# Performance work log

Measured on AMD Instinct MI355X. Metric: run time of the kernel, lower is better.

Reference implementation:

```python
import jax, jax.numpy as jnp
import numpy as np

H, NOPE, ROPE, VDIM, LORA = 16, 128, 64, 128, 512
DM, T, S, K = 2048, 256, 32768, 2048
SCALE = 1.0 / np.sqrt(NOPE + ROPE)
ROPE_BASE = 10000.0


def _rope(x, pos):
    # x: [..., D] with rotary dim D; pos broadcastable to x[..., :1] leading dims
    d = x.shape[-1]
    half = d // 2
    inv = 1.0 / (ROPE_BASE ** (jnp.arange(half, dtype=jnp.float32) / half))
    f = pos[..., None].astype(jnp.float32) * inv  # [..., half]
    cos, sin = jnp.cos(f), jnp.sin(f)
    x1, x2 = x[..., :half], x[..., half:]
    return jnp.concatenate([x1 * cos - x2 * sin, x2 * cos + x1 * sin], axis=-1)


def setup_inputs() -> dict:
    key = jax.random.key(0)
    ks = jax.random.split(key, 9)
    return {
        "x": jax.random.normal(ks[0], (T, DM), jnp.float32) * 0.02,
        "Wq": jax.random.normal(ks[1], (DM, H * (NOPE + ROPE)), jnp.float32) * 0.02,
        "W_UK": jax.random.normal(ks[2], (H, NOPE, LORA), jnp.float32) * 0.02,
        "W_UV": jax.random.normal(ks[3], (H, VDIM, LORA), jnp.float32) * 0.02,
        "Wo": jax.random.normal(ks[4], (H * VDIM, DM), jnp.float32) * 0.02,
        "kv_c": jax.random.normal(ks[5], (S, LORA), jnp.float32),
        "k_pe": jax.random.normal(ks[6], (S, ROPE), jnp.float32),
        "topk_indices": jnp.sort(jax.random.randint(ks[7], (T, K), 0, S, jnp.int32), axis=-1),
        "pos_q": jax.random.randint(ks[8], (T,), 0, S, jnp.int32),
    }


def reference(x, Wq, W_UK, W_UV, Wo, kv_c, k_pe, topk_indices, pos_q):
    n_tok = x.shape[0]
    # q projection -> [T, H, nope+rope], split (MLAAttention._q_proj_and_k_up_proj)
    q = (x @ Wq).reshape(n_tok, H, NOPE + ROPE)
    q_nope, q_pe = q[..., :NOPE], q[..., NOPE:]
    # absorbed k up-projection: q_nope @ W_UK -> latent space [T, H, LORA]
    ql_nope = jnp.einsum("thn,hnl->thl", q_nope, W_UK)
    # rotary on rope parts
    q_pe = _rope(q_pe, pos_q[:, None])            # [T, H, ROPE]
    k_pe_r = _rope(k_pe, jnp.arange(k_pe.shape[0]))  # [S, ROPE]
    # top-k sparse KV gather (DSA indexer / triton index conversion)
    kv_sel = kv_c[topk_indices]                    # [T, K, LORA]
    kpe_sel = k_pe_r[topk_indices]                 # [T, K, ROPE]
    # attention scores in latent space over selected tokens
    scores = (jnp.einsum("thl,tkl->thk", ql_nope, kv_sel)
              + jnp.einsum("thr,tkr->thk", q_pe, kpe_sel)) * SCALE
    attn = jax.nn.softmax(scores, axis=-1)         # [T, H, K]
    o_lat = jnp.einsum("thk,tkl->thl", attn, kv_sel)  # [T, H, LORA]
    # v up-projection (_v_up_proj_and_o_proj) then output proj
    ov = jnp.einsum("thl,hvl->thv", o_lat, W_UV).reshape(n_tok, H * VDIM)
    return ov @ Wo
```

## Files before the change

kernel.cpp:

```cpp
#include <hip/hip_runtime.h>
#include <hip/hip_bf16.h>

#define H_    16
#define NOPE_ 128
#define ROPE_ 64
#define VDIM_ 128
#define LORA_ 512
#define DM_   2048
#define T_    256
#define S_    32768
#define K_    2048

static constexpr float SCALE_ = 0.072168783648703220563643597562744f;
static constexpr float LOG2E_ = 1.4426950408889634f;

typedef __attribute__((ext_vector_type(8))) short short8;
typedef __attribute__((ext_vector_type(4))) short short4v;
typedef __attribute__((ext_vector_type(4))) float f32x4;

__device__ __forceinline__ ushort f2bf(float f) {
    unsigned u = __float_as_uint(f);
    unsigned r = (u + 0x7FFFu + ((u >> 16) & 1u)) >> 16;
    return (ushort)r;
}
__device__ __forceinline__ float bf2f(ushort u) {
    return __uint_as_float((unsigned)u << 16);
}

template<bool A_BF16, bool B_NT, bool C_BF16, bool SMALL_M>
__global__ __launch_bounds__(256) void gemm_mfma(
    const void* __restrict__ Av, const float* __restrict__ B, void* __restrict__ Cv,
    int M, int N, int Kd, int lda, int ldb, int ldc,
    long batchA, long batchB, long batchC)
{
    constexpr int BM = SMALL_M ? 32 : 64;
    constexpr int MT = SMALL_M ? 1 : 2;
    __shared__ ushort As[64 * 72];
    __shared__ ushort Bs[64 * 72];

    const int tid = threadIdx.x;
    const int w  = tid >> 6;
    const int l  = tid & 63;
    const int lm = l & 15;
    const int kq = l >> 4;
    const int bm = blockIdx.y * BM;
    const int bn = blockIdx.x * 64;
    const int m0 = SMALL_M ? (w >> 1) * 16 : (w >> 1) * 32;
    const int n0 = (w & 1) * 32;

    const float*  Af = A_BF16 ? nullptr : ((const float*)Av)  + (long)blockIdx.z * batchA;
    const ushort* Ah = A_BF16 ? ((const ushort*)Av) + (long)blockIdx.z * batchA : nullptr;
    B += (long)blockIdx.z * batchB;

    f32x4 acc[MT][2];
    #pragma unroll
    for (int i = 0; i < MT; ++i)
        #pragma unroll
        for (int j = 0; j < 2; ++j) acc[i][j] = (f32x4){0.f, 0.f, 0.f, 0.f};

    const int am  = SMALL_M ? (tid >> 3) : (tid >> 2);
    const int ako = SMALL_M ? (tid & 7) * 8 : (tid & 3) * 16;
    const int amr = SMALL_M ? (tid >> 3) : (tid >> 4);
    const int akk = SMALL_M ? (tid & 7) * 8 : (tid & 15) * 4;
    const int bnr = tid >> 4, bkk = (tid & 15) * 4;
    const int bk  = tid >> 2, bnq = (tid & 3) * 16;

    uint4  gA[2];
    float4 gAf[4];
    float4 gB[4];

    auto loadA = [&](int k0) {
        if constexpr (A_BF16) {
            const ushort* src = Ah + (long)(bm + am) * lda + k0 + ako;
            gA[0] = *(const uint4*)(src);
            if constexpr (!SMALL_M) gA[1] = *(const uint4*)(src + 8);
        } else {
            if constexpr (SMALL_M) {
                const float* s = Af + (long)(bm + amr) * lda + k0 + akk;
                gAf[0] = *(const float4*)s;
                gAf[1] = *(const float4*)(s + 4);
            } else {
                #pragma unroll
                for (int p = 0; p < 4; ++p)
                    gAf[p] = *(const float4*)(Af + (long)(bm + amr + p * 16) * lda + k0 + akk);
            }
        }
    };
    auto loadB = [&](int k0) {
        if constexpr (B_NT) {
            #pragma unroll
            for (int p = 0; p < 4; ++p)
                gB[p] = *(const float4*)(B + (long)(bn + bnr + p * 16) * ldb + k0 + bkk);
        } else {
            #pragma unroll
            for (int p = 0; p < 4; ++p)
                gB[p] = *(const float4*)(B + (long)(k0 + bk) * ldb + bn + bnq + p * 4);
        }
    };

    loadA(0); loadB(0);

    for (int k0 = 0; k0 < Kd; k0 += 64) {
        __syncthreads();
        if constexpr (A_BF16) {
            *(uint4*)(As + am * 72 + ako) = gA[0];
            if constexpr (!SMALL_M)
                *(uint4*)(As + am * 72 + ako + 8) = gA[1];
        } else {
            if constexpr (SMALL_M) {
                ushort4 u0, u1;
                u0.x = f2bf(gAf[0].x); u0.y = f2bf(gAf[0].y);
                u0.z = f2bf(gAf[0].z); u0.w = f2bf(gAf[0].w);
                u1.x = f2bf(gAf[1].x); u1.y = f2bf(gAf[1].y);
                u1.z = f2bf(gAf[1].z); u1.w = f2bf(gAf[1].w);
                *(ushort4*)(As + amr * 72 + akk)     = u0;
                *(ushort4*)(As + amr * 72 + akk + 4) = u1;
            } else {
                #pragma unroll
                for (int p = 0; p < 4; ++p) {
                    ushort4 u;
                    u.x = f2bf(gAf[p].x); u.y = f2bf(gAf[p].y);
                    u.z = f2bf(gAf[p].z); u.w = f2bf(gAf[p].w);
                    *(ushort4*)(As + (amr + p * 16) * 72 + akk) = u;
                }
            }
        }
        if constexpr (B_NT) {
            #pragma unroll
            for (int p = 0; p < 4; ++p) {
                ushort4 u;
                u.x = f2bf(gB[p].x); u.y = f2bf(gB[p].y);
                u.z = f2bf(gB[p].z); u.w = f2bf(gB[p].w);
                *(ushort4*)(Bs + (bnr + p * 16) * 72 + bkk) = u;
            }
        } else {
            #pragma unroll
            for (int p = 0; p < 4; ++p) {
                ushort4 u;
                u.x = f2bf(gB[p].x); u.y = f2bf(gB[p].y);
                u.z = f2bf(gB[p].z); u.w = f2bf(gB[p].w);
                *(ushort4*)(Bs + bk * 68 + bnq + p * 4) = u;
            }
        }
        if (k0 + 64 < Kd) { loadA(k0 + 64); loadB(k0 + 64); }
        __syncthreads();
        #pragma unroll
        for (int ks = 0; ks < 2; ++ks) {
            short8 a[MT], b[2];
            #pragma unroll
            for (int mt = 0; mt < MT; ++mt)
                a[mt] = *(const short8*)(As + (m0 + mt * 16 + lm) * 72 + ks * 32 + kq * 8);
            if constexpr (B_NT) {
                #pragma unroll
                for (int nt = 0; nt < 2; ++nt)
                    b[nt] = *(const short8*)(Bs + (n0 + nt * 16 + lm) * 72 + ks * 32 + kq * 8);
            } else {
                #pragma unroll
                for (int nt = 0; nt < 2; ++nt)
                    #pragma unroll
                    for (int j = 0; j < 8; ++j)
                        b[nt][j] = (short)Bs[(ks * 32 + kq * 8 + j) * 68 + n0 + nt * 16 + lm];
            }
            #pragma unroll
            for (int mt = 0; mt < MT; ++mt)
                #pragma unroll
                for (int nt = 0; nt < 2; ++nt)
                    acc[mt][nt] = __builtin_amdgcn_mfma_f32_16x16x32_bf16(
                        a[mt], b[nt], acc[mt][nt], 0, 0, 0);
        }
    }
    #pragma unroll
    for (int mt = 0; mt < MT; ++mt)
        #pragma unroll
        for (int nt = 0; nt < 2; ++nt)
            #pragma unroll
            for (int r = 0; r < 4; ++r) {
                long row = bm + m0 + mt * 16 + kq * 4 + r;
                long col = bn + n0 + nt * 16 + lm;
                if constexpr (C_BF16)
                    ((ushort*)Cv)[(long)blockIdx.z * batchC + row * ldc + col] =
                        f2bf(acc[mt][nt][r]);
                else
                    ((float*)Cv)[(long)blockIdx.z * batchC + row * ldc + col] =
                        acc[mt][nt][r];
            }
}

__global__ __launch_bounds__(256) void pack_qrope(
    const float* __restrict__ qfull, const int* __restrict__ pos_q,
    ushort* __restrict__ qb)
{
    int id = blockIdx.x * 256 + threadIdx.x;
    int i = id & 31;
    int h = (id >> 5) & 15;
    int t = id >> 9;
    double inv = exp2(-(double)i * 0.41524101186092026);
    double f = (double)pos_q[t] * inv;
    double fr = f - floor(f * 0.15915494309189535) * 6.283185307179586;
    float sf, cf;
    sincosf((float)fr, &sf, &cf);
    float x1 = qfull[t * 3072 + h * 192 + 128 + i];
    float x2 = qfull[t * 3072 + h * 192 + 160 + i];
    ushort* q = qb + (long)(t * 16 + h) * 576;
    q[512 + i] = f2bf(x1 * cf - x2 * sf);
    q[544 + i] = f2bf(x2 * cf + x1 * sf);
}

__global__ __launch_bounds__(256) void prep_kvb(
    const float* __restrict__ kvc, const float* __restrict__ kpe,
    ushort* __restrict__ kvb)
{
    int id = blockIdx.x * 256 + threadIdx.x;
    int s = id / 96;
    int c = id - s * 96;
    if (c < 64) {
        const float* src = kvc + (long)s * 512 + c * 8;
        float4 v0 = *(const float4*)src;
        float4 v1 = *(const float4*)(src + 4);
        ushort4 a, b;
        a.x = f2bf(v0.x); a.y = f2bf(v0.y); a.z = f2bf(v0.z); a.w = f2bf(v0.w);
        b.x = f2bf(v1.x); b.y = f2bf(v1.y); b.z = f2bf(v1.z); b.w = f2bf(v1.w);
        ushort* dst = kvb + (long)s * 576 + c * 8;
        *(ushort4*)dst = a;
        *(ushort4*)(dst + 4) = b;
    } else {
        int i = c - 64;
        double inv = exp2(-(double)i * 0.41524101186092026);
        double f = (double)s * inv;
        double fr = f - floor(f * 0.15915494309189535) * 6.283185307179586;
        float sf, cf;
        sincosf((float)fr, &sf, &cf);
        const float* kp = kpe + (long)s * 64;
        float x1 = kp[i], x2 = kp[32 + i];
        ushort* dst = kvb + (long)s * 576 + 512;
        dst[i]      = f2bf(x1 * cf - x2 * sf);
        dst[32 + i] = f2bf(x2 * cf + x1 * sf);
    }
}

#define KBD 2048
#define KBSZ 73728

__global__ __launch_bounds__(256, 4) void mla_fused_split(
    const ushort* __restrict__ qb, const ushort* __restrict__ kvb,
    const int* __restrict__ topk,
    ushort* __restrict__ Opart, float* __restrict__ ml)
{
    __shared__ __align__(16) char kb[KBSZ];
    __shared__ __align__(16) ushort P2[1024];
    __shared__ float wred[2][4][16];

    const int t = blockIdx.x;
    const int sp = blockIdx.y;
    const int tid = threadIdx.x;
    const int w = tid >> 6;
    const int l = tid & 63;
    const int lm = l & 15;
    const int kq = l >> 4;

    short8 qa[18];
    {
        const ushort* qrow = qb + (long)(t * 16 + lm) * 576 + kq * 8;
        #pragma unroll
        for (int ks = 0; ks < 18; ++ks)
            qa[ks] = *(const short8*)(qrow + ks * 32);
    }

    const int* tkp = topk + (long)t * 2048 + sp * 1024;

    const int kh   = w & 1;
    const int db0  = w >> 1;
    const int skey = 32 * kh + (l >> 1);
    const int gcol = db0 * 16 + (l & 1) * 8;
    const unsigned stRel = (unsigned)(db0 * 2048 + kh * 1024);

    __attribute__((address_space(3))) char* kb3 =
        (__attribute__((address_space(3))) char*)&kb[0];
    const char* kbg = (const char*)&kb[0];
    const unsigned kbBase = (unsigned)(unsigned long long)(const void*)&kb[0];

    const unsigned krowRel = (unsigned)((kq >> 1) * KBD + w * 512 + (lm >> 2) * 128
                     + (lm & 3) * 32 + (kq & 1) * 16);
    const unsigned trb = kbBase + (unsigned)(w * 8 * KBD + kq * 256 + lm * 8);
    const unsigned ptrb = (unsigned)(unsigned long long)(const void*)P2
                        + (unsigned)(kq * 256 + lm * 8);

    f32x4 O[8];
    #pragma unroll
    for (int vt = 0; vt < 8; ++vt) O[vt] = (f32x4){0.f, 0.f, 0.f, 0.f};
    float m_r[4] = {-1e30f, -1e30f, -1e30f, -1e30f};
    float l_r[4] = {0.f, 0.f, 0.f, 0.f};

#define GSTAGE(IDX)                                                           \
    {                                                                         \
        const ushort* gs = kvb + (long)(IDX) * 576 + gcol;                    \
        _Pragma("unroll")                                                     \
        for (int i = 0; i < 18; ++i)                                          \
            __builtin_amdgcn_global_load_lds(                                 \
                (const __attribute__((address_space(1))) void*)(const void*)(gs + i * 32), \
                (__attribute__((address_space(3))) void*)(kb3 + stRel + i * 4096), \
                16, 0, 0);                                                    \
    }

    for (int tt = 0; tt < 16; ++tt) {
        int idx = tkp[tt * 64 + skey];
        __syncthreads();
        GSTAGE(idx)

        const char* krow = kbg + krowRel;
        f32x4 S0 = (f32x4){0.f, 0.f, 0.f, 0.f};
        f32x4 S1 = (f32x4){0.f, 0.f, 0.f, 0.f};

        asm volatile("s_waitcnt vmcnt(12)" ::: "memory");
        __builtin_amdgcn_s_barrier();
        asm volatile("" ::: "memory");
        #pragma unroll
        for (int ks = 0; ks < 6; ks += 2) {
            short8 b0 = *(const short8*)(krow + ks * (2 * KBD));
            S0 = __builtin_amdgcn_mfma_f32_16x16x32_bf16(qa[ks], b0, S0, 0, 0, 0);
            short8 b1 = *(const short8*)(krow + (ks + 1) * (2 * KBD));
            S1 = __builtin_amdgcn_mfma_f32_16x16x32_bf16(qa[ks + 1], b1, S1, 0, 0, 0);
        }
        asm volatile("s_waitcnt vmcnt(6)" ::: "memory");
        __builtin_amdgcn_s_barrier();
        asm volatile("" ::: "memory");
        #pragma unroll
        for (int ks = 6; ks < 12; ks += 2) {
            short8 b0 = *(const short8*)(krow + ks * (2 * KBD));
            S0 = __builtin_amdgcn_mfma_f32_16x16x32_bf16(qa[ks], b0, S0, 0, 0, 0);
            short8 b1 = *(const short8*)(krow + (ks + 1) * (2 * KBD));
            S1 = __builtin_amdgcn_mfma_f32_16x16x32_bf16(qa[ks + 1], b1, S1, 0, 0, 0);
        }
        asm volatile("s_waitcnt vmcnt(0)" ::: "memory");
        __builtin_amdgcn_s_barrier();
        asm volatile("" ::: "memory");
        #pragma unroll
        for (int ks = 12; ks < 18; ks += 2) {
            short8 b0 = *(const short8*)(krow + ks * (2 * KBD));
            S0 = __builtin_amdgcn_mfma_f32_16x16x32_bf16(qa[ks], b0, S0, 0, 0, 0);
            short8 b1 = *(const short8*)(krow + (ks + 1) * (2 * KBD));
            S1 = __builtin_amdgcn_mfma_f32_16x16x32_bf16(qa[ks + 1], b1, S1, 0, 0, 0);
        }

        float s4[4], mx[4], p[4];
        #pragma unroll
        for (int r = 0; r < 4; ++r) { s4[r] = (S0[r] + S1[r]) * SCALE_; mx[r] = s4[r]; }
        #pragma unroll
        for (int off = 1; off < 16; off <<= 1)
            #pragma unroll
            for (int r = 0; r < 4; ++r)
                mx[r] = fmaxf(mx[r], __shfl_xor(mx[r], off, 64));
        if (lm == 0)
            #pragma unroll
            for (int r = 0; r < 4; ++r) wred[0][w][4 * kq + r] = mx[r];
        asm volatile("s_waitcnt lgkmcnt(0)" ::: "memory");
        __builtin_amdgcn_s_barrier();
        asm volatile("" ::: "memory");

        float al[4], rs[4];
        #pragma unroll
        for (int r = 0; r < 4; ++r) {
            float tm = fmaxf(fmaxf(wred[0][0][4 * kq + r], wred[0][1][4 * kq + r]),
                             fmaxf(wred[0][2][4 * kq + r], wred[0][3][4 * kq + r]));
            float mn = fmaxf(m_r[r], tm);
            al[r] = exp2f((m_r[r] - mn) * LOG2E_);
            p[r] = exp2f((s4[r] - mn) * LOG2E_);
            m_r[r] = mn;
            rs[r] = p[r];
        }
        #pragma unroll
        for (int off = 1; off < 16; off <<= 1)
            #pragma unroll
            for (int r = 0; r < 4; ++r)
                rs[r] += __shfl_xor(rs[r], off, 64);
        if (lm == 0)
            #pragma unroll
            for (int r = 0; r < 4; ++r) wred[1][w][4 * kq + r] = rs[r];
        {
            ushort4 pu;
            pu.x = f2bf(p[0]); pu.y = f2bf(p[1]);
            pu.z = f2bf(p[2]); pu.w = f2bf(p[3]);
            *(ushort4*)(P2 + (w * 4 + (lm >> 2)) * 64 + (lm & 3) * 16 + 4 * kq) = pu;
        }
        #pragma unroll
        for (int vt = 0; vt < 8; ++vt)
            #pragma unroll
            for (int r = 0; r < 4; ++r)
                O[vt][r] *= al[r];
        asm volatile("s_waitcnt lgkmcnt(0)" ::: "memory");
        __builtin_amdgcn_s_barrier();
        asm volatile("" ::: "memory");

        #pragma unroll
        for (int r = 0; r < 4; ++r) {
            float ts = wred[1][0][4 * kq + r] + wred[1][1][4 * kq + r] +
                       wred[1][2][4 * kq + r] + wred[1][3][4 * kq + r];
            l_r[r] = l_r[r] * al[r] + ts;
        }

        __builtin_amdgcn_sched_barrier(0);
        short4v pr[4];
        asm volatile("ds_read_b64_tr_b16 %0, %1 offset:0"    : "=v"(pr[0]) : "v"(ptrb));
        asm volatile("ds_read_b64_tr_b16 %0, %1 offset:128"  : "=v"(pr[1]) : "v"(ptrb));
        asm volatile("ds_read_b64_tr_b16 %0, %1 offset:1024" : "=v"(pr[2]) : "v"(ptrb));
        asm volatile("ds_read_b64_tr_b16 %0, %1 offset:1152" : "=v"(pr[3]) : "v"(ptrb));
        short4v rg[2][4];
#define ISSUE_V(vt, slot) \
        asm volatile("ds_read_b64_tr_b16 %0, %1 offset:%2" : "=v"(rg[slot][0]) : "v"(trb), "i"((vt) * KBD));        \
        asm volatile("ds_read_b64_tr_b16 %0, %1 offset:%2" : "=v"(rg[slot][1]) : "v"(trb), "i"((vt) * KBD + 128));  \
        asm volatile("ds_read_b64_tr_b16 %0, %1 offset:%2" : "=v"(rg[slot][2]) : "v"(trb), "i"((vt) * KBD + 1024)); \
        asm volatile("ds_read_b64_tr_b16 %0, %1 offset:%2" : "=v"(rg[slot][3]) : "v"(trb), "i"((vt) * KBD + 1152));
        ISSUE_V(0, 0)
        ISSUE_V(1, 1)
        asm volatile("s_waitcnt lgkmcnt(8)" ::: "memory");
        __builtin_amdgcn_sched_barrier(0);
        short8 pa0 = __builtin_shufflevector(pr[0], pr[1], 0, 1, 2, 3, 4, 5, 6, 7);
        short8 pa1 = __builtin_shufflevector(pr[2], pr[3], 0, 1, 2, 3, 4, 5, 6, 7);
        #pragma unroll
        for (int vt = 0; vt < 8; ++vt) {
            if (vt < 7)
                asm volatile("s_waitcnt lgkmcnt(4)" ::: "memory");
            else
                asm volatile("s_waitcnt lgkmcnt(0)" ::: "memory");
            __builtin_amdgcn_sched_barrier(0);
            short8 bv0 = __builtin_shufflevector(rg[vt & 1][0], rg[vt & 1][1],
                                                 0, 1, 2, 3, 4, 5, 6, 7);
            O[vt] = __builtin_amdgcn_mfma_f32_16x16x32_bf16(pa0, bv0, O[vt], 0, 0, 0);
            short8 bv1 = __builtin_shufflevector(rg[vt & 1][2], rg[vt & 1][3],
                                                 0, 1, 2, 3, 4, 5, 6, 7);
            O[vt] = __builtin_amdgcn_mfma_f32_16x16x32_bf16(pa1, bv1, O[vt], 0, 0, 0);
            if (vt < 6) { ISSUE_V(vt + 2, vt & 1) }
        }
#undef ISSUE_V
    }

    const long rbase = ((long)sp * 256 + t) * 16;
    #pragma unroll
    for (int vt = 0; vt < 8; ++vt)
        #pragma unroll
        for (int r = 0; r < 4; ++r)
            Opart[(rbase + 4 * kq + r) * 512 + w * 128 + vt * 16 + lm] = f2bf(O[vt][r]);
    if (w == 0 && lm == 0) {
        #pragma unroll
        for (int r = 0; r < 4; ++r) {
            ml[(rbase + 4 * kq + r) * 2 + 0] = m_r[r];
            ml[(rbase + 4 * kq + r) * 2 + 1] = l_r[r];
        }
    }
#undef GSTAGE
}

__global__ __launch_bounds__(256) void combine_kernel(
    const ushort* __restrict__ Opart, const float* __restrict__ ml,
    ushort* __restrict__ olat)
{
    const int t = blockIdx.x;
    const int h = threadIdx.x >> 4;
    const int v0 = (threadIdx.x & 15) * 32;
    const long r0 = (long)t * 16 + h;
    const long r1 = (long)(256 + t) * 16 + h;
    float m0 = ml[r0 * 2], l0 = ml[r0 * 2 + 1];
    float m1 = ml[r1 * 2], l1 = ml[r1 * 2 + 1];
    float M = fmaxf(m0, m1);
    float w0 = exp2f((m0 - M) * LOG2E_);
    float w1 = exp2f((m1 - M) * LOG2E_);
    float inv = 1.0f / (w0 * l0 + w1 * l1);
    const ushort* p0 = Opart + r0 * 512 + v0;
    const ushort* p1 = Opart + r1 * 512 + v0;
    ushort* po = olat + r0 * 512 + v0;
    #pragma unroll
    for (int i = 0; i < 32; i += 4) {
        ushort4 a = *(const ushort4*)(p0 + i);
        ushort4 b = *(const ushort4*)(p1 + i);
        ushort4 o;
        o.x = f2bf((w0 * bf2f(a.x) + w1 * bf2f(b.x)) * inv);
        o.y = f2bf((w0 * bf2f(a.y) + w1 * bf2f(b.y)) * inv);
        o.z = f2bf((w0 * bf2f(a.z) + w1 * bf2f(b.z)) * inv);
        o.w = f2bf((w0 * bf2f(a.w) + w1 * bf2f(b.w)) * inv);
        *(ushort4*)(po + i) = o;
    }
}

extern "C" void kernel_launch(void* const* d_in, const int* in_sizes, int n_in,
                              void* d_out, int out_size, void* d_ws, size_t ws_size,
                              hipStream_t stream)
{
    const float* x    = (const float*)d_in[0];
    const float* Wq   = (const float*)d_in[1];
    const float* W_UK = (const float*)d_in[2];
    const float* W_UV = (const float*)d_in[3];
    const float* Wo   = (const float*)d_in[4];
    const float* kv_c = (const float*)d_in[5];
    const float* k_pe = (const float*)d_in[6];
    const int* topk   = (const int*)d_in[7];
    const int* pos_q  = (const int*)d_in[8];
    float* out        = (float*)d_out;

    char* wsb = (char*)d_ws;
    ushort* qb    = (ushort*)wsb;
    float*  qfull = (float*)(wsb + 4718592);
    ushort* Opart = (ushort*)(wsb + 4718592);
    ushort* ov_b  = (ushort*)(wsb + 13107200);
    float*  ml    = (float*)(wsb + 14155776);
    ushort* olat  = qb;
    ushort* kvb   = (ushort*)(wsb + 16252928);
    if (ws_size < (size_t)54001664) return;

    prep_kvb<<<12288, 256, 0, stream>>>(kv_c, k_pe, kvb);

    gemm_mfma<false, false, false, true><<<dim3(48, 8), 256, 0, stream>>>(
        x, Wq, qfull, 256, 3072, 2048, 2048, 3072, 3072, 0, 0, 0);

    gemm_mfma<false, false, true, false><<<dim3(8, 4, 16), 256, 0, stream>>>(
        qfull, W_UK, qb, 256, 512, 128, 3072, 512, 9216, 192, 65536, 576);

    pack_qrope<<<512, 256, 0, stream>>>(qfull, pos_q, qb);

    mla_fused_split<<<dim3(256, 2), 256, 0, stream>>>(qb, kvb, topk, Opart, ml);

    combine_kernel<<<256, 256, 0, stream>>>(Opart, ml, olat);

    gemm_mfma<true, true, true, true><<<dim3(2, 8, 16), 256, 0, stream>>>(
        olat, W_UV, ov_b, 256, 128, 512, 8192, 512, 2048, 512, 65536, 128);

    gemm_mfma<true, false, false, true><<<dim3(32, 8), 256, 0, stream>>>(
        ov_b, Wo, out, 256, 2048, 2048, 2048, 2048, 2048, 0, 0, 0);
}
```

Baseline: 311.6 us.

## Double-buffer GEMM register prefetch, add setprio around MFMA, lazy softmax rescale

The generic GEMM now uses two register prefetch sets and unrolls the K loop by two. This lets global loads for the tile two steps ahead overlap with compute on the current tile. The attention kernel wraps its MFMA bursts in s_setprio to favour matrix work across waves. Its online softmax also skips the running-max update and O rescale when every row's new max stays within a threshold of the old one. That last change alters the numerics: the exponent can reach up to 2^(8·log2e) before normalisation, and the GEMM loop assumes Kd is a multiple of 128.

Measured after the change: 312.5 us. About the same (+0.3%).

```diff
diff --git a/kernel.cpp b/kernel.cpp
--- a/kernel.cpp
+++ b/kernel.cpp
@@ -65,110 +65,126 @@
     const int bnr = tid >> 4, bkk = (tid & 15) * 4;
     const int bk  = tid >> 2, bnq = (tid & 3) * 16;
 
-    uint4  gA[2];
-    float4 gAf[4];
-    float4 gB[4];
-
-    auto loadA = [&](int k0) {
-        if constexpr (A_BF16) {
-            const ushort* src = Ah + (long)(bm + am) * lda + k0 + ako;
-            gA[0] = *(const uint4*)(src);
-            if constexpr (!SMALL_M) gA[1] = *(const uint4*)(src + 8);
-        } else {
-            if constexpr (SMALL_M) {
-                const float* s = Af + (long)(bm + amr) * lda + k0 + akk;
-                gAf[0] = *(const float4*)s;
-                gAf[1] = *(const float4*)(s + 4);
-            } else {
-                #pragma unroll
-                for (int p = 0; p < 4; ++p)
-                    gAf[p] = *(const float4*)(Af + (long)(bm + amr + p * 16) * lda + k0 + akk);
-            }
-        }
-    };
-    auto loadB = [&](int k0) {
-        if constexpr (B_NT) {
-            #pragma unroll
-            for (int p = 0; p < 4; ++p)
-                gB[p] = *(const float4*)(B + (long)(bn + bnr + p * 16) * ldb + k0 + bkk);
-        } else {
-            #pragma unroll
-            for (int p = 0; p < 4; ++p)
-                gB[p] = *(const float4*)(B + (long)(k0 + bk) * ldb + bn + bnq + p * 4);
-        }
-    };
-
-    loadA(0); loadB(0);
-
-    for (int k0 = 0; k0 < Kd; k0 += 64) {
+    uint4  gAx[2], gAy[2];
+    float4 gAfx[4], gAfy[4];
+    float4 gBx[4], gBy[4];
+
+#define LOADA(GA, GAF, K0) {                                                  \
+        if constexpr (A_BF16) {                                               \
+            const ushort* src = Ah + (long)(bm + am) * lda + (K0) + ako;      \
+            GA[0] = *(const uint4*)(src);                                     \
+            if constexpr (!SMALL_M) GA[1] = *(const uint4*)(src + 8);         \
+        } else if constexpr (SMALL_M) {                                       \
+            const float* s = Af + (long)(bm + amr) * lda + (K0) + akk;        \
+            GAF[0] = *(const float4*)s;                                       \
+            GAF[1] = *(const float4*)(s + 4);                                 \
+        } else {                                                              \
+            _Pragma("unroll")                                                 \
+            for (int p = 0; p < 4; ++p)                                       \
+                GAF[p] = *(const float4*)(Af + (long)(bm + amr + p * 16) * lda + (K0) + akk); \
+        }                                                                     \
+    }
+#define LOADB(GB, K0) {                                                       \
+        if constexpr (B_NT) {                                                 \
+            _Pragma("unroll")                                                 \
+            for (int p = 0; p < 4; ++p)                                       \
+                GB[p] = *(const float4*)(B + (long)(bn + bnr + p * 16) * ldb + (K0) + bkk); \
+        } else {                                                              \
+            _Pragma("unroll")                                                 \
+            for (int p = 0; p < 4; ++p)                                       \
+                GB[p] = *(const float4*)(B + (long)((K0) + bk) * ldb + bn + bnq + p * 4); \
+        }                                                                     \
+    }
+#define STOREA(GA, GAF) {                                                     \
+        if constexpr (A_BF16) {                                               \
+            *(uint4*)(As + am * 72 + ako) = GA[0];                            \
+            if constexpr (!SMALL_M)                                           \
+                *(uint4*)(As + am * 72 + ako + 8) = GA[1];                    \
+        } else if constexpr (SMALL_M) {                                       \
+            ushort4 u0, u1;                                                   \
+            u0.x = f2bf(GAF[0].x); u0.y = f2bf(GAF[0].y);                     \
+            u0.z = f2bf(GAF[0].z); u0.w = f2bf(GAF[0].w);                     \
+            u1.x = f2bf(GAF[1].x); u1.y = f2bf(GAF[1].y);                     \
+            u1.z = f2bf(GAF[1].z); u1.w = f2bf(GAF[1].w);                     \
+            *(ushort4*)(As + amr * 72 + akk)     = u0;                        \
+            *(ushort4*)(As + amr * 72 + akk + 4) = u1;                        \
+        } else {                                                              \
+            _Pragma("unroll")                                                 \
+            for (int p = 0; p < 4; ++p) {                                     \
+                ushort4 u;                                                    \
+                u.x = f2bf(GAF[p].x); u.y = f2bf(GAF[p].y);                   \
+                u.z = f2bf(GAF[p].z); u.w = f2bf(GAF[p].w);                   \
+                *(ushort4*)(As + (amr + p * 16) * 72 + akk) = u;              \
+            }                                                                 \
+        }                                                                     \
+    }
+#define STOREB(GB) {                                                          \
+        if constexpr (B_NT) {                                                 \
+            _Pragma("unroll")                                                 \
+            for (int p = 0; p < 4; ++p) {                                     \
+                ushort4 u;                                                    \
+                u.x = f2bf(GB[p].x); u.y = f2bf(GB[p].y);                     \
+                u.z = f2bf(GB[p].z); u.w = f2bf(GB[p].w);                     \
+                *(ushort4*)(Bs + (bnr + p * 16) * 72 + bkk) = u;              \
+            }                                                                 \
+        } else {                                                              \
+            _Pragma("unroll")                                                 \
+            for (int p = 0; p < 4; ++p) {                                     \
+                ushort4 u;                                                    \
+                u.x = f2bf(GB[p].x); u.y = f2bf(GB[p].y);                     \
+                u.z = f2bf(GB[p].z); u.w = f2bf(GB[p].w);                     \
+                *(ushort4*)(Bs + bk * 68 + bnq + p * 4) = u;                  \
+            }                                                                 \
+        }                                                                     \
+    }
+#define COMPUTE {                                                             \
+        _Pragma("unroll")                                                     \
+        for (int ks = 0; ks < 2; ++ks) {                                      \
+            short8 a[MT], b[2];                                               \
+            _Pragma("unroll")                                                 \
+            for (int mt = 0; mt < MT; ++mt)                                   \
+                a[mt] = *(const short8*)(As + (m0 + mt * 16 + lm) * 72 + ks * 32 + kq * 8); \
+            if constexpr (B_NT) {                                             \
+                _Pragma("unroll")                                             \
+                for (int nt = 0; nt < 2; ++nt)                                \
+                    b[nt] = *(const short8*)(Bs + (n0 + nt * 16 + lm) * 72 + ks * 32 + kq * 8); \
+            } else {                                                          \
+                _Pragma("unroll")                                             \
+                for (int nt = 0; nt < 2; ++nt)                                \
+                    _Pragma("unroll")                                         \
+                    for (int j = 0; j < 8; ++j)                               \
+                        b[nt][j] = (short)Bs[(ks * 32 + kq * 8 + j) * 68 + n0 + nt * 16 + lm]; \
+            }                                                                 \
+            _Pragma("unroll")                                                 \
+            for (int mt = 0; mt < MT; ++mt)                                   \
+                _Pragma("unroll")                                             \
+                for (int nt = 0; nt < 2; ++nt)                                \
+                    acc[mt][nt] = __builtin_amdgcn_mfma_f32_16x16x32_bf16(    \
+                        a[mt], b[nt], acc[mt][nt], 0, 0, 0);                  \
+        }                                                                     \
+    }
+
+    LOADA(gAx, gAfx, 0) LOADB(gBx, 0)
+    LOADA(gAy, gAfy, 64) LOADB(gBy, 64)
+
+    for (int k0 = 0; k0 < Kd; k0 += 128) {
         __syncthreads();
-        if constexpr (A_BF16) {
-            *(uint4*)(As + am * 72 + ako) = gA[0];
-            if constexpr (!SMALL_M)
-                *(uint4*)(As + am * 72 + ako + 8) = gA[1];
-        } else {
-            if constexpr (SMALL_M) {
-                ushort4 u0, u1;
-                u0.x = f2bf(gAf[0].x); u0.y = f2bf(gAf[0].y);
-                u0.z = f2bf(gAf[0].z); u0.w = f2bf(gAf[0].w);
-                u1.x = f2bf(gAf[1].x); u1.y = f2bf(gAf[1].y);
-                u1.z = f2bf(gAf[1].z); u1.w = f2bf(gAf[1].w);
-                *(ushort4*)(As + amr * 72 + akk)     = u0;
-                *(ushort4*)(As + amr * 72 + akk + 4) = u1;
-            } else {
-                #pragma unroll
-                for (int p = 0; p < 4; ++p) {
-                    ushort4 u;
-                    u.x = f2bf(gAf[p].x); u.y = f2bf(gAf[p].y);
-                    u.z = f2bf(gAf[p].z); u.w = f2bf(gAf[p].w);
-                    *(ushort4*)(As + (amr + p * 16) * 72 + akk) = u;
-                }
-            }
-        }
-        if constexpr (B_NT) {
-            #pragma unroll
-            for (int p = 0; p < 4; ++p) {
-                ushort4 u;
-                u.x = f2bf(gB[p].x); u.y = f2bf(gB[p].y);
-                u.z = f2bf(gB[p].z); u.w = f2bf(gB[p].w);
-                *(ushort4*)(Bs + (bnr + p * 16) * 72 + bkk) = u;
-            }
-        } else {
-            #pragma unroll
-            for (int p = 0; p < 4; ++p) {
-                ushort4 u;
-                u.x = f2bf(gB[p].x); u.y = f2bf(gB[p].y);
-                u.z = f2bf(gB[p].z); u.w = f2bf(gB[p].w);
-                *(ushort4*)(Bs + bk * 68 + bnq + p * 4) = u;
-            }
-        }
-        if (k0 + 64 < Kd) { loadA(k0 + 64); loadB(k0 + 64); }
+        STOREA(gAx, gAfx) STOREB(gBx)
+        if (k0 + 128 < Kd) { LOADA(gAx, gAfx, k0 + 128) LOADB(gBx, k0 + 128) }
         __syncthreads();
-        #pragma unroll
-        for (int ks = 0; ks < 2; ++ks) {
-            short8 a[MT], b[2];
-            #pragma unroll
-            for (int mt = 0; mt < MT; ++mt)
-                a[mt] = *(const short8*)(As + (m0 + mt * 16 + lm) * 72 + ks * 32 + kq * 8);
-            if constexpr (B_NT) {
-                #pragma unroll
-                for (int nt = 0; nt < 2; ++nt)
-                    b[nt] = *(const short8*)(Bs + (n0 + nt * 16 + lm) * 72 + ks * 32 + kq * 8);
-            } else {
-                #pragma unroll
-                for (int nt = 0; nt < 2; ++nt)
-                    #pragma unroll
-                    for (int j = 0; j < 8; ++j)
-                        b[nt][j] = (short)Bs[(ks * 32 + kq * 8 + j) * 68 + n0 + nt * 16 + lm];
-            }
-            #pragma unroll
-            for (int mt = 0; mt < MT; ++mt)
-                #pragma unroll
-                for (int nt = 0; nt < 2; ++nt)
-                    acc[mt][nt] = __builtin_amdgcn_mfma_f32_16x16x32_bf16(
-                        a[mt], b[nt], acc[mt][nt], 0, 0, 0);
-        }
-    }
+        COMPUTE
+        __syncthreads();
+        STOREA(gAy, gAfy) STOREB(gBy)
+        if (k0 + 192 < Kd) { LOADA(gAy, gAfy, k0 + 192) LOADB(gBy, k0 + 192) }
+        __syncthreads();
+        COMPUTE
+    }
+#undef LOADA
+#undef LOADB
+#undef STOREA
+#undef STOREB
+#undef COMPUTE
+
     #pragma unroll
     for (int mt = 0; mt < MT; ++mt)
         #pragma unroll
@@ -314,6 +330,7 @@
         asm volatile("s_waitcnt vmcnt(12)" ::: "memory");
         __builtin_amdgcn_s_barrier();
         asm volatile("" ::: "memory");
+        __builtin_amdgcn_s_setprio(1);
         #pragma unroll
         for (int ks = 0; ks < 6; ks += 2) {
             short8 b0 = *(const short8*)(krow + ks * (2 * KBD));
@@ -321,9 +338,11 @@
             short8 b1 = *(const short8*)(krow + (ks + 1) * (2 * KBD));
             S1 = __builtin_amdgcn_mfma_f32_16x16x32_bf16(qa[ks + 1], b1, S1, 0, 0, 0);
         }
+        __builtin_amdgcn_s_setprio(0);
         asm volatile("s_waitcnt vmcnt(6)" ::: "memory");
         __builtin_amdgcn_s_barrier();
         asm volatile("" ::: "memory");
+        __builtin_amdgcn_s_setprio(1);
         #pragma unroll
         for (int ks = 6; ks < 12; ks += 2) {
             short8 b0 = *(const short8*)(krow + ks * (2 * KBD));
@@ -331,9 +350,11 @@
             short8 b1 = *(const short8*)(krow + (ks + 1) * (2 * KBD));
             S1 = __builtin_amdgcn_mfma_f32_16x16x32_bf16(qa[ks + 1], b1, S1, 0, 0, 0);
         }
+        __builtin_amdgcn_s_setprio(0);
         asm volatile("s_waitcnt vmcnt(0)" ::: "memory");
         __builtin_amdgcn_s_barrier();
         asm volatile("" ::: "memory");
+        __builtin_amdgcn_s_setprio(1);
         #pragma unroll
         for (int ks = 12; ks < 18; ks += 2) {
             short8 b0 = *(const short8*)(krow + ks * (2 * KBD));
@@ -341,8 +362,9 @@
             short8 b1 = *(const short8*)(krow + (ks + 1) * (2 * KBD));
             S1 = __builtin_amdgcn_mfma_f32_16x16x32_bf16(qa[ks + 1], b1, S1, 0, 0, 0);
         }
-
-        float s4[4], mx[4], p[4];
+        __builtin_amdgcn_s_setprio(0);
+
+        float s4[4], mx[4];
         #pragma unroll
         for (int r = 0; r < 4; ++r) { s4[r] = (S0[r] + S1[r]) * SCALE_; mx[r] = s4[r]; }
         #pragma unroll
@@ -357,16 +379,30 @@
         __builtin_amdgcn_s_barrier();
         asm volatile("" ::: "memory");
 
-        float al[4], rs[4];
-        #pragma unroll
-        for (int r = 0; r < 4; ++r) {
-            float tm = fmaxf(fmaxf(wred[0][0][4 * kq + r], wred[0][1][4 * kq + r]),
-                             fmaxf(wred[0][2][4 * kq + r], wred[0][3][4 * kq + r]));
-            float mn = fmaxf(m_r[r], tm);
-            al[r] = exp2f((m_r[r] - mn) * LOG2E_);
-            p[r] = exp2f((s4[r] - mn) * LOG2E_);
-            m_r[r] = mn;
-            rs[r] = p[r];
+        float tm[4], al[4], p[4], rs[4];
+        #pragma unroll
+        for (int r = 0; r < 4; ++r)
+            tm[r] = fmaxf(fmaxf(wred[0][0][4 * kq + r], wred[0][1][4 * kq + r]),
+                          fmaxf(wred[0][2][4 * kq + r], wred[0][3][4 * kq + r]));
+        bool okl = (tm[0] <= m_r[0] + 8.0f) && (tm[1] <= m_r[1] + 8.0f) &&
+                   (tm[2] <= m_r[2] + 8.0f) && (tm[3] <= m_r[3] + 8.0f);
+        const bool skip = __all(okl);
+        if (skip) {
+            #pragma unroll
+            for (int r = 0; r < 4; ++r) {
+                al[r] = 1.0f;
+                p[r] = exp2f((s4[r] - m_r[r]) * LOG2E_);
+                rs[r] = p[r];
+            }
+        } else {
+            #pragma unroll
+            for (int r = 0; r < 4; ++r) {
+                float mn = fmaxf(m_r[r], tm[r]);
+                al[r] = exp2f((m_r[r] - mn) * LOG2E_);
+                p[r] = exp2f((s4[r] - mn) * LOG2E_);
+                m_r[r] = mn;
+                rs[r] = p[r];
+            }
         }
         #pragma unroll
         for (int off = 1; off < 16; off <<= 1)
@@ -382,11 +418,13 @@
             pu.z = f2bf(p[2]); pu.w = f2bf(p[3]);
             *(ushort4*)(P2 + (w * 4 + (lm >> 2)) * 64 + (lm & 3) * 16 + 4 * kq) = pu;
         }
-        #pragma unroll
-        for (int vt = 0; vt < 8; ++vt)
-            #pragma unroll
-            for (int r = 0; r < 4; ++r)
-                O[vt][r] *= al[r];
+        if (!skip) {
+            #pragma unroll
+            for (int vt = 0; vt < 8; ++vt)
+                #pragma unroll
+                for (int r = 0; r < 4; ++r)
+                    O[vt][r] *= al[r];
+        }
         asm volatile("s_waitcnt lgkmcnt(0)" ::: "memory");
         __builtin_amdgcn_s_barrier();
         asm volatile("" ::: "memory");
@@ -423,12 +461,14 @@
             else
                 asm volatile("s_waitcnt lgkmcnt(0)" ::: "memory");
             __builtin_amdgcn_sched_barrier(0);
+            __builtin_amdgcn_s_setprio(1);
             short8 bv0 = __builtin_shufflevector(rg[vt & 1][0], rg[vt & 1][1],
                                                  0, 1, 2, 3, 4, 5, 6, 7);
             O[vt] = __builtin_amdgcn_mfma_f32_16x16x32_bf16(pa0, bv0, O[vt], 0, 0, 0);
             short8 bv1 = __builtin_shufflevector(rg[vt & 1][2], rg[vt & 1][3],
                                                  0, 1, 2, 3, 4, 5, 6, 7);
             O[vt] = __builtin_amdgcn_mfma_f32_16x16x32_bf16(pa1, bv1, O[vt], 0, 0, 0);
+            __builtin_amdgcn_s_setprio(0);
             if (vt < 6) { ISSUE_V(vt + 2, vt & 1) }
         }
 #undef ISSUE_V
```
